# Performance work log

Hardware: AMD Instinct MI355X
Metric: run time of the kernel (lower is better)

## Reference

```python
import jax, jax.numpy as jnp
import numpy as np

N_HEAD_FULL = 16  # config.n_head

def setup_inputs() -> dict:
    key = jax.random.key(0)
    ks = jax.random.split(key, 5)
    B, T, D = 2, 2048, 2048
    s = 0.02
    return {
        "x": jax.random.normal(ks[0], (B, T, D), dtype=jnp.float32),
        "Wq": jax.random.normal(ks[1], (D, D), dtype=jnp.float32) * s,
        "Wk": jax.random.normal(ks[2], (D, D), dtype=jnp.float32) * s,
        "Wv": jax.random.normal(ks[3], (D, D), dtype=jnp.float32) * s,
        "Wo": jax.random.normal(ks[4], (D, D), dtype=jnp.float32) * s,
        "active_dim": 1024,
        "active_kv": 64,
    }

def reference(x, Wq, Wk, Wv, Wo, active_dim, active_kv):
    B, T, D = x.shape
    d = active_dim if active_dim is not None else D
    head_dim_base = D // N_HEAD_FULL          # 128
    kv_dim = active_kv if active_kv is not None else head_dim_base
    n_head = d // head_dim_base               # active heads
    head_dim = d // n_head                    # == head_dim_base

    xs = x[..., :d]                            # [B,T,d]
    # F.linear(x, W[:d,:d]) == x @ W[:d,:d].T
    q = jnp.einsum('btc,dc->btd', xs, Wq[:d, :d])
    k = jnp.einsum('btc,dc->btd', xs, Wk[:d, :d])
    v = jnp.einsum('btc,dc->btd', xs, Wv[:d, :d])

    def split_heads(t):  # [B,T,d] -> [B,h,T,hd]
        return t.reshape(B, T, n_head, head_dim).transpose(0, 2, 1, 3)
    q, k, v = split_heads(q), split_heads(k), split_heads(v)

    if kv_dim < head_dim:
        q, k, v = q[..., :kv_dim], k[..., :kv_dim], v[..., :kv_dim]

    scale = 1.0 / np.sqrt(kv_dim).astype(np.float32)
    attn = jnp.einsum('bhqd,bhkd->bhqk', q, k) * scale  # [B,h,T,T]
    causal = jnp.tril(jnp.ones((T, T), dtype=bool))
    attn = jnp.where(causal, attn, jnp.float32(-jnp.inf))
    attn = jax.nn.softmax(attn, axis=-1)
    out = jnp.einsum('bhqk,bhkd->bhqd', attn, v)        # [B,h,T,kv]

    if kv_dim < head_dim:
        out = jnp.pad(out, ((0, 0), (0, 0), (0, 0), (0, head_dim - kv_dim)))
    out = out.transpose(0, 2, 1, 3).reshape(B, T, d)
    out = jnp.einsum('btc,dc->btd', out, Wo[:d, :d])
    if d < D:
        out = jnp.pad(out, ((0, 0), (0, 0), (0, D - d)))
    return out
```

## Files before the change

kernel.cpp:

```cpp
#include <hip/hip_runtime.h>
#include <hip/hip_bf16.h>

typedef __attribute__((ext_vector_type(8))) short bf16x8;
typedef __attribute__((ext_vector_type(4))) float f32x4;

#define MFMA16(a,b,c) __builtin_amdgcn_mfma_f32_16x16x32_bf16((a),(b),(c),0,0,0)

static __device__ __forceinline__ unsigned short f2bf(float f) {
    unsigned int u = __builtin_bit_cast(unsigned int, f);
    u += 0x7fffu + ((u >> 16) & 1u);
    return (unsigned short)(u >> 16);
}

static __device__ __forceinline__ void g2l16(const unsigned short* g, unsigned short* l) {
    __builtin_amdgcn_global_load_lds(
        (const __attribute__((address_space(1))) unsigned int*)g,
        (__attribute__((address_space(3))) unsigned int*)l,
        16, 0, 0);
}

#define BT     4096
#define DFULL  2048
#define DACT   1024
#define DKV    64
#define NSEL   512
#define TSEQ   2048
#define PADR   72

__global__ __launch_bounds__(256) void prep_kernel(
    const float* __restrict__ x,  const float* __restrict__ Wq,
    const float* __restrict__ Wk, const float* __restrict__ Wv,
    const float* __restrict__ Wo,
    unsigned short* __restrict__ xb,  unsigned short* __restrict__ Wqb,
    unsigned short* __restrict__ Wkb, unsigned short* __restrict__ Wvb,
    unsigned short* __restrict__ Wob)
{
    const int NA = (BT * DACT) / 8;
    const int NB = (NSEL * DACT) / 8;
    const int NC = (DACT * NSEL) / 8;
    const int TOT = NA + 3 * NB + NC;
    for (int u = blockIdx.x * blockDim.x + threadIdx.x; u < TOT;
         u += gridDim.x * blockDim.x) {
        if (u < NA) {
            int e = u * 8; int row = e >> 10, col = e & 1023;
            const float* s = x + (size_t)row * DFULL + col;
            f32x4 v0 = *(const f32x4*)s, v1 = *(const f32x4*)(s + 4);
            bf16x8 o;
            #pragma unroll
            for (int j = 0; j < 4; ++j) { o[j] = (short)f2bf(v0[j]); o[4+j] = (short)f2bf(v1[j]); }
            *(bf16x8*)(xb + e) = o;
        } else if (u < NA + 3 * NB) {
            int t = u - NA; int mat = t / NB; int q = t % NB;
            int e = q * 8; int n = e >> 10, c = e & 1023;
            const float* W = (mat == 0) ? Wq : (mat == 1) ? Wk : Wv;
            unsigned short* Wb = (mat == 0) ? Wqb : (mat == 1) ? Wkb : Wvb;
            int wrow = (n >> 6) * 128 + (n & 63);
            const float* s = W + (size_t)wrow * DFULL + c;
            f32x4 v0 = *(const f32x4*)s, v1 = *(const f32x4*)(s + 4);
            bf16x8 o;
            #pragma unroll
            for (int j = 0; j < 4; ++j) { o[j] = (short)f2bf(v0[j]); o[4+j] = (short)f2bf(v1[j]); }
            *(bf16x8*)(Wb + e) = o;
        } else {
            int q = u - NA - 3 * NB;
            int e = q * 8; int r = e >> 9, cs = e & 511;
            int col = (cs >> 6) * 128 + (cs & 63);
            const float* s = Wo + (size_t)r * DFULL + col;
            f32x4 v0 = *(const f32x4*)s, v1 = *(const f32x4*)(s + 4);
            bf16x8 o;
            #pragma unroll
            for (int j = 0; j < 4; ++j) { o[j] = (short)f2bf(v0[j]); o[4+j] = (short)f2bf(v1[j]); }
            *(bf16x8*)(Wob + e) = o;
        }
    }
}

__global__ __launch_bounds__(256) void qkv_gemm(
    const unsigned short* __restrict__ xb,
    const unsigned short* __restrict__ Wall,
    unsigned short* __restrict__ Qb, unsigned short* __restrict__ Kb,
    unsigned short* __restrict__ Vtb)
{
    __shared__ unsigned short As[64 * 64];
    __shared__ unsigned short Bs[128 * 64];
    const int m0 = blockIdx.y * 64, n0 = blockIdx.x * 128;
    const int tid = threadIdx.x, w = tid >> 6, l = tid & 63;
    const int lr = l & 15, g = l >> 4, lk = g * 8;
    const int wr = w >> 1, wc = w & 1;
    const int srow = l >> 3, scol = (l & 7) * 8;

    f32x4 acc[2][4] = {};
    for (int k0 = 0; k0 < DACT; k0 += 64) {
        __syncthreads();
        #pragma unroll
        for (int i = 0; i < 2; ++i) {
            int chunk = w * 2 + i;
            int row = chunk * 8 + srow;
            g2l16(&xb[(size_t)(m0 + row) * DACT + k0 + scol], &As[chunk * 512]);
        }
        #pragma unroll
        for (int i = 0; i < 4; ++i) {
            int chunk = w * 4 + i;
            int row = chunk * 8 + srow;
            g2l16(&Wall[(size_t)(n0 + row) * DACT + k0 + scol], &Bs[chunk * 512]);
        }
        __syncthreads();
        #pragma unroll
        for (int kk = 0; kk < 64; kk += 32) {
            bf16x8 a[2], b[4];
            #pragma unroll
            for (int m = 0; m < 2; ++m)
                a[m] = *(const bf16x8*)&As[(wr * 32 + m * 16 + lr) * 64 + kk + lk];
            #pragma unroll
            for (int n = 0; n < 4; ++n)
                b[n] = *(const bf16x8*)&Bs[(wc * 64 + n * 16 + lr) * 64 + kk + lk];
            #pragma unroll
            for (int m = 0; m < 2; ++m)
                #pragma unroll
                for (int n = 0; n < 4; ++n)
                    acc[m][n] = MFMA16(a[m], b[n], acc[m][n]);
        }
    }
    #pragma unroll
    for (int m = 0; m < 2; ++m)
        #pragma unroll
        for (int n = 0; n < 4; ++n)
            #pragma unroll
            for (int i = 0; i < 4; ++i) {
                int row = m0 + wr * 32 + m * 16 + g * 4 + i;
                int col = n0 + wc * 64 + n * 16 + lr;
                int mat = col >> 9, r = col & 511, h = r >> 6, j = r & 63;
                int bb = row >> 11, t = row & 2047, bh = bb * 8 + h;
                float v = acc[m][n][i];
                if (mat == 0)
                    Qb[((size_t)bh * TSEQ + t) * DKV + j] = f2bf(v * 0.125f);
                else if (mat == 1)
                    Kb[((size_t)bh * TSEQ + t) * DKV + (j ^ ((t & 7) << 3))] = f2bf(v);
                else
                    Vtb[(((size_t)bh * 32 + (t >> 6)) * 64 + j) * 64 +
                        ((t & 63) ^ ((j & 7) << 3))] = f2bf(v);
            }
}

__global__ __launch_bounds__(512, 4) void attn_kernel(
    const unsigned short* __restrict__ Qb,
    const unsigned short* __restrict__ Kb,
    const unsigned short* __restrict__ Vtb,
    unsigned short* __restrict__ att)
{
    __shared__ unsigned short KV[2][2][2][4096];
    __shared__ unsigned short Ps[8][16 * 64];
    const int f = blockIdx.x;
    const int k = f & 255, bh = k & 15, pi = k >> 4;
    const int S = (f < 256) ? (31 - pi) : pi;
    const int ntt = S + 1;
    const int np = (ntt + 1) >> 1;
    const int tid = threadIdx.x, w = tid >> 6, l = tid & 63;
    const int lr = l & 15, g = l >> 4, lk = g * 8;
    const int s = w >> 1, j = w & 1;
    const size_t kvb = (size_t)bh * TSEQ * DKV;
    const int bb = bh >> 3, h = bh & 7;
    const int qs0 = S * 64 + s * 16;

    unsigned short* Psw = Ps[w];
    const short os = (short)0x3F80;
    const bf16x8 ones = {os, os, os, os, os, os, os, os};

    bf16x8 qf0 = *(const bf16x8*)&Qb[kvb + (size_t)(qs0 + lr) * DKV + lk];
    bf16x8 qf1 = *(const bf16x8*)&Qb[kvb + (size_t)(qs0 + lr) * DKV + 32 + lk];

    f32x4 acc[4] = {};
    f32x4 dacc = {};

    #define STAGE(b, p)                                                        \
        do {                                                                   \
            int r_ = w >> 1, par_ = r_ >> 1, kv_ = r_ & 1;                     \
            int t_ = 2 * (p) + par_;                                           \
            if (t_ < ntt) {                                                    \
                const unsigned short* src_ =                                   \
                    (kv_ ? Vtb : Kb) + kvb + (size_t)t_ * 4096 + (w & 1) * 2048; \
                unsigned short* dst_ = &KV[b][par_][kv_][(w & 1) * 2048];      \
                g2l16(&src_[l * 8],        dst_);                              \
                g2l16(&src_[512 + l * 8],  dst_ + 512);                        \
                g2l16(&src_[1024 + l * 8], dst_ + 1024);                       \
                g2l16(&src_[1536 + l * 8], dst_ + 1536);                       \
            }                                                                  \
        } while (0)

    STAGE(0, 0);
    __syncthreads();

    for (int p = 0; p < np; ++p) {
        const int cur = p & 1;
        if (p + 1 < np) STAGE(cur ^ 1, p + 1);

        const int jt = 2 * p + j;
        if (jt < ntt) {
            const unsigned short* Kt = KV[cur][j][0];
            const unsigned short* Vt = KV[cur][j][1];

            #pragma unroll
            for (int c = 0; c < 4; ++c) {
                const int row = c * 16 + lr, sr = (row & 7) << 3;
                bf16x8 b0 = *(const bf16x8*)&Kt[row * 64 + (lk ^ sr)];
                bf16x8 b1 = *(const bf16x8*)&Kt[row * 64 + ((32 + lk) ^ sr)];
                f32x4 z = {};
                z = MFMA16(qf0, b0, z);
                z = MFMA16(qf1, b1, z);
                if (jt == ntt - 1) {
                    int kcol = jt * 64 + c * 16 + lr;
                    #pragma unroll
                    for (int i = 0; i < 4; ++i)
                        if (kcol > qs0 + g * 4 + i) z[i] = -64.f;
                }
                const int colp = c * 16 + lr;
                #pragma unroll
                for (int i = 0; i < 4; ++i) {
                    const int prow = g * 4 + i;
                    Psw[prow * 64 + (colp ^ ((prow & 7) << 3))] =
                        f2bf(__expf(z[i]));
                }
            }
            const int psr = (lr & 7) << 3;
            bf16x8 pa0 = *(const bf16x8*)&Psw[lr * 64 + (lk ^ psr)];
            bf16x8 pa1 = *(const bf16x8*)&Psw[lr * 64 + ((32 + lk) ^ psr)];

            #pragma unroll
            for (int n = 0; n < 4; ++n) {
                const int row = n * 16 + lr, sr = (row & 7) << 3;
                bf16x8 v0 = *(const bf16x8*)&Vt[row * 64 + (lk ^ sr)];
                bf16x8 v1 = *(const bf16x8*)&Vt[row * 64 + ((32 + lk) ^ sr)];
                acc[n] = MFMA16(pa0, v0, acc[n]);
                acc[n] = MFMA16(pa1, v1, acc[n]);
            }
            dacc = MFMA16(pa0, ones, dacc);
            dacc = MFMA16(pa1, ones, dacc);
        }
        __syncthreads();
    }
    #undef STAGE

    float* M = (float*)KV;
    if (j == 1) {
        #pragma unroll
        for (int n = 0; n < 4; ++n)
            #pragma unroll
            for (int i = 0; i < 4; ++i)
                M[s * 1088 + (g * 4 + i) * 64 + n * 16 + lr] = acc[n][i];
        if (lr == 0) {
            #pragma unroll
            for (int i = 0; i < 4; ++i)
                M[s * 1088 + 1024 + g * 4 + i] = dacc[i];
        }
    }
    __syncthreads();
    if (j == 0) {
        #pragma unroll
        for (int i = 0; i < 4; ++i) {
            float den = dacc[i] + M[s * 1088 + 1024 + g * 4 + i];
            float inv = 1.0f / den;
            int t = qs0 + g * 4 + i;
            #pragma unroll
            for (int n = 0; n < 4; ++n) {
                float v = acc[n][i] + M[s * 1088 + (g * 4 + i) * 64 + n * 16 + lr];
                att[((size_t)bb * TSEQ + t) * NSEL + h * 64 + n * 16 + lr] =
                    f2bf(v * inv);
            }
        }
    }
}

__global__ __launch_bounds__(256) void oproj_gemm(
    const unsigned short* __restrict__ att,
    const unsigned short* __restrict__ Wob,
    float* __restrict__ out)
{
    const int tid = threadIdx.x;
    if (blockIdx.x >= 8) {
        const int m0z = blockIdx.y * 128;
        const int n0z = DACT + (blockIdx.x - 8) * 128;
        const f32x4 z = {0.f, 0.f, 0.f, 0.f};
        #pragma unroll
        for (int i = 0; i < 16; ++i) {
            int chunk = tid + i * 256;
            int row = chunk >> 5, c = (chunk & 31) * 4;
            *(f32x4*)&out[(size_t)(m0z + row) * DFULL + n0z + c] = z;
        }
        return;
    }
    __shared__ unsigned short As[128 * 64];
    __shared__ unsigned short Bs[128 * 64];
    const int m0 = blockIdx.y * 128, n0 = blockIdx.x * 128;
    const int w = tid >> 6, l = tid & 63;
    const int lr = l & 15, g = l >> 4, lk = g * 8;
    const int wr = w >> 1, wc = w & 1;
    const int srow = l >> 3, scol = (l & 7) * 8;

    f32x4 acc[4][4] = {};
    for (int k0 = 0; k0 < NSEL; k0 += 64) {
        __syncthreads();
        #pragma unroll
        for (int i = 0; i < 4; ++i) {
            int chunk = w * 4 + i;
            int row = chunk * 8 + srow;
            g2l16(&att[(size_t)(m0 + row) * NSEL + k0 + scol], &As[chunk * 512]);
            g2l16(&Wob[(size_t)(n0 + row) * NSEL + k0 + scol], &Bs[chunk * 512]);
        }
        __syncthreads();
        #pragma unroll
        for (int kk = 0; kk < 64; kk += 32) {
            bf16x8 a[4], b[4];
            #pragma unroll
            for (int m = 0; m < 4; ++m)
                a[m] = *(const bf16x8*)&As[(wr * 64 + m * 16 + lr) * 64 + kk + lk];
            #pragma unroll
            for (int n = 0; n < 4; ++n)
                b[n] = *(const bf16x8*)&Bs[(wc * 64 + n * 16 + lr) * 64 + kk + lk];
            #pragma unroll
            for (int m = 0; m < 4; ++m)
                #pragma unroll
                for (int n = 0; n < 4; ++n)
                    acc[m][n] = MFMA16(a[m], b[n], acc[m][n]);
        }
    }
    #pragma unroll
    for (int m = 0; m < 4; ++m)
        #pragma unroll
        for (int n = 0; n < 4; ++n)
            #pragma unroll
            for (int i = 0; i < 4; ++i) {
                int row = m0 + wr * 64 + m * 16 + g * 4 + i;
                int col = n0 + wc * 64 + n * 16 + lr;
                out[(size_t)row * DFULL + col] = acc[m][n][i];
            }
}

extern "C" void kernel_launch(void* const* d_in, const int* in_sizes, int n_in,
                              void* d_out, int out_size, void* d_ws, size_t ws_size,
                              hipStream_t stream) {
    const float* x  = (const float*)d_in[0];
    const float* Wq = (const float*)d_in[1];
    const float* Wk = (const float*)d_in[2];
    const float* Wv = (const float*)d_in[3];
    const float* Wo = (const float*)d_in[4];
    float* out = (float*)d_out;

    char* ws = (char*)d_ws;
    unsigned short* xb  = (unsigned short*)(ws);
    unsigned short* Wqb = (unsigned short*)(ws + 8388608);
    unsigned short* Wkb = (unsigned short*)(ws + 9437184);
    unsigned short* Wvb = (unsigned short*)(ws + 10485760);
    unsigned short* Wob = (unsigned short*)(ws + 11534336);
    unsigned short* Qb  = (unsigned short*)(ws + 12582912);
    unsigned short* Kb  = (unsigned short*)(ws + 16777216);
    unsigned short* Vtb = (unsigned short*)(ws + 20971520);
    unsigned short* att = (unsigned short*)(ws + 25165824);

    prep_kernel<<<2048, 256, 0, stream>>>(x, Wq, Wk, Wv, Wo,
                                          xb, Wqb, Wkb, Wvb, Wob);
    qkv_gemm<<<dim3(12, 64), 256, 0, stream>>>(xb, Wqb, Qb, Kb, Vtb);
    attn_kernel<<<512, 512, 0, stream>>>(Qb, Kb, Vtb, att);
    oproj_gemm<<<dim3(16, 32), 256, 0, stream>>>(att, Wob, out);
}
```

Baseline: 82.57 us.

## Halve attention query tile to 32 rows with 4-wave blocks

Splits each attention block's 64-row query tile into two 32-row tiles run by 256-thread blocks, doubling the grid to 1024 blocks. Each wave now stages a full K or V tile through two LDS halves, and the compute loops pick the half by row. The aim is better load balance and occupancy across CUs for the causal triangle. The cost is that K/V tiles are streamed from memory twice as often per query row.

```diff
diff --git a/kernel.cpp b/kernel.cpp
--- a/kernel.cpp
+++ b/kernel.cpp
@@ -142,25 +142,26 @@
             }
 }
 
-__global__ __launch_bounds__(512, 4) void attn_kernel(
+__global__ __launch_bounds__(256, 4) void attn_kernel(
     const unsigned short* __restrict__ Qb,
     const unsigned short* __restrict__ Kb,
     const unsigned short* __restrict__ Vtb,
     unsigned short* __restrict__ att)
 {
-    __shared__ unsigned short KV[2][2][2][4096];
-    __shared__ unsigned short Ps[8][16 * 64];
+    __shared__ unsigned short KV[2][2][2][2048];
+    __shared__ unsigned short KV2[2][2][2][2048];
+    __shared__ unsigned short Ps[4][16 * 64];
     const int f = blockIdx.x;
-    const int k = f & 255, bh = k & 15, pi = k >> 4;
-    const int S = (f < 256) ? (31 - pi) : pi;
-    const int ntt = S + 1;
+    const int k = f & 511, bh = k & 15, pi = k >> 4;
+    const int Q = (f < 512) ? (63 - pi) : pi;
+    const int ntt = (Q >> 1) + 1;
     const int np = (ntt + 1) >> 1;
     const int tid = threadIdx.x, w = tid >> 6, l = tid & 63;
     const int lr = l & 15, g = l >> 4, lk = g * 8;
     const int s = w >> 1, j = w & 1;
     const size_t kvb = (size_t)bh * TSEQ * DKV;
     const int bb = bh >> 3, h = bh & 7;
-    const int qs0 = S * 64 + s * 16;
+    const int qs0 = Q * 32 + s * 16;
 
     unsigned short* Psw = Ps[w];
     const short os = (short)0x3F80;
@@ -174,16 +175,21 @@
 
     #define STAGE(b, p)                                                        \
         do {                                                                   \
-            int r_ = w >> 1, par_ = r_ >> 1, kv_ = r_ & 1;                     \
+            int par_ = w >> 1, kv_ = w & 1;                                    \
             int t_ = 2 * (p) + par_;                                           \
             if (t_ < ntt) {                                                    \
                 const unsigned short* src_ =                                   \
-                    (kv_ ? Vtb : Kb) + kvb + (size_t)t_ * 4096 + (w & 1) * 2048; \
-                unsigned short* dst_ = &KV[b][par_][kv_][(w & 1) * 2048];      \
-                g2l16(&src_[l * 8],        dst_);                              \
-                g2l16(&src_[512 + l * 8],  dst_ + 512);                        \
-                g2l16(&src_[1024 + l * 8], dst_ + 1024);                       \
-                g2l16(&src_[1536 + l * 8], dst_ + 1536);                       \
+                    (kv_ ? Vtb : Kb) + kvb + (size_t)t_ * 4096;                \
+                unsigned short* d0_ = KV[b][par_][kv_];                        \
+                unsigned short* d1_ = KV2[b][par_][kv_];                       \
+                g2l16(&src_[l * 8],        d0_);                               \
+                g2l16(&src_[512 + l * 8],  d0_ + 512);                         \
+                g2l16(&src_[1024 + l * 8], d0_ + 1024);                        \
+                g2l16(&src_[1536 + l * 8], d0_ + 1536);                        \
+                g2l16(&src_[2048 + l * 8], d1_);                               \
+                g2l16(&src_[2560 + l * 8], d1_ + 512);                         \
+                g2l16(&src_[3072 + l * 8], d1_ + 1024);                        \
+                g2l16(&src_[3584 + l * 8], d1_ + 1536);                        \
             }                                                                  \
         } while (0)
 
@@ -196,14 +202,18 @@
 
         const int jt = 2 * p + j;
         if (jt < ntt) {
-            const unsigned short* Kt = KV[cur][j][0];
-            const unsigned short* Vt = KV[cur][j][1];
+            const unsigned short* Kt0 = KV[cur][j][0];
+            const unsigned short* Kt1 = KV2[cur][j][0];
+            const unsigned short* Vt0 = KV[cur][j][1];
+            const unsigned short* Vt1 = KV2[cur][j][1];
 
             #pragma unroll
             for (int c = 0; c < 4; ++c) {
                 const int row = c * 16 + lr, sr = (row & 7) << 3;
-                bf16x8 b0 = *(const bf16x8*)&Kt[row * 64 + (lk ^ sr)];
-                bf16x8 b1 = *(const bf16x8*)&Kt[row * 64 + ((32 + lk) ^ sr)];
+                const unsigned short* Kt = (row < 32) ? Kt0 : Kt1;
+                const int rrow = row & 31;
+                bf16x8 b0 = *(const bf16x8*)&Kt[rrow * 64 + (lk ^ sr)];
+                bf16x8 b1 = *(const bf16x8*)&Kt[rrow * 64 + ((32 + lk) ^ sr)];
                 f32x4 z = {};
                 z = MFMA16(qf0, b0, z);
                 z = MFMA16(qf1, b1, z);
@@ -228,8 +238,10 @@
             #pragma unroll
             for (int n = 0; n < 4; ++n) {
                 const int row = n * 16 + lr, sr = (row & 7) << 3;
-                bf16x8 v0 = *(const bf16x8*)&Vt[row * 64 + (lk ^ sr)];
-                bf16x8 v1 = *(const bf16x8*)&Vt[row * 64 + ((32 + lk) ^ sr)];
+                const unsigned short* Vt = (row < 32) ? Vt0 : Vt1;
+                const int rrow = row & 31;
+                bf16x8 v0 = *(const bf16x8*)&Vt[rrow * 64 + (lk ^ sr)];
+                bf16x8 v1 = *(const bf16x8*)&Vt[rrow * 64 + ((32 + lk) ^ sr)];
                 acc[n] = MFMA16(pa0, v0, acc[n]);
                 acc[n] = MFMA16(pa1, v1, acc[n]);
             }
@@ -359,6 +371,6 @@
     prep_kernel<<<2048, 256, 0, stream>>>(x, Wq, Wk, Wv, Wo,
                                           xb, Wqb, Wkb, Wvb, Wob);
     qkv_gemm<<<dim3(12, 64), 256, 0, stream>>>(xb, Wqb, Qb, Kb, Vtb);
-    attn_kernel<<<512, 512, 0, stream>>>(Qb, Kb, Vtb, att);
+    attn_kernel<<<1024, 256, 0, stream>>>(Qb, Kb, Vtb, att);
     oproj_gemm<<<dim3(16, 32), 256, 0, stream>>>(att, Wob, out);
 }
```

New measurement: 93.56 us. +13.3%, slower.

## Split attention blocks into 32-row query tiles and drop LDS double buffering

Applied to the files above, without the earlier changes.

The attention kernel now launches 1024 blocks of 256 threads, each covering 32 query rows instead of 64, so there are twice as many smaller blocks. The LDS K/V double buffer becomes a single buffer, loaded synchronously each iteration with barriers before and after the load. This halves LDS per block, which should let more blocks fit per CU and spread the causal workload more evenly. The cost is that K/V tiles are reloaded by twice as many blocks, and load latency is no longer overlapped with compute.

```diff
diff --git a/kernel.cpp b/kernel.cpp
--- a/kernel.cpp
+++ b/kernel.cpp
@@ -142,25 +142,25 @@
             }
 }
 
-__global__ __launch_bounds__(512, 4) void attn_kernel(
+__global__ __launch_bounds__(256, 4) void attn_kernel(
     const unsigned short* __restrict__ Qb,
     const unsigned short* __restrict__ Kb,
     const unsigned short* __restrict__ Vtb,
     unsigned short* __restrict__ att)
 {
-    __shared__ unsigned short KV[2][2][2][4096];
-    __shared__ unsigned short Ps[8][16 * 64];
+    __shared__ unsigned short KV[2][2][4096];
+    __shared__ unsigned short Ps[4][16 * 64];
     const int f = blockIdx.x;
-    const int k = f & 255, bh = k & 15, pi = k >> 4;
-    const int S = (f < 256) ? (31 - pi) : pi;
-    const int ntt = S + 1;
+    const int k = f & 511, bh = k & 15, pi = k >> 4;
+    const int Q = (f < 512) ? (63 - pi) : pi;
+    const int ntt = (Q >> 1) + 1;
     const int np = (ntt + 1) >> 1;
     const int tid = threadIdx.x, w = tid >> 6, l = tid & 63;
     const int lr = l & 15, g = l >> 4, lk = g * 8;
     const int s = w >> 1, j = w & 1;
     const size_t kvb = (size_t)bh * TSEQ * DKV;
     const int bb = bh >> 3, h = bh & 7;
-    const int qs0 = S * 64 + s * 16;
+    const int qs0 = Q * 32 + s * 16;
 
     unsigned short* Psw = Ps[w];
     const short os = (short)0x3F80;
@@ -172,32 +172,34 @@
     f32x4 acc[4] = {};
     f32x4 dacc = {};
 
-    #define STAGE(b, p)                                                        \
+    #define STAGE(p)                                                           \
         do {                                                                   \
-            int r_ = w >> 1, par_ = r_ >> 1, kv_ = r_ & 1;                     \
+            int par_ = w >> 1, kv_ = w & 1;                                    \
             int t_ = 2 * (p) + par_;                                           \
             if (t_ < ntt) {                                                    \
                 const unsigned short* src_ =                                   \
-                    (kv_ ? Vtb : Kb) + kvb + (size_t)t_ * 4096 + (w & 1) * 2048; \
-                unsigned short* dst_ = &KV[b][par_][kv_][(w & 1) * 2048];      \
-                g2l16(&src_[l * 8],        dst_);                              \
-                g2l16(&src_[512 + l * 8],  dst_ + 512);                        \
-                g2l16(&src_[1024 + l * 8], dst_ + 1024);                       \
-                g2l16(&src_[1536 + l * 8], dst_ + 1536);                       \
+                    (kv_ ? Vtb : Kb) + kvb + (size_t)t_ * 4096;                \
+                unsigned short* d_ = KV[par_][kv_];                            \
+                g2l16(&src_[l * 8],        d_);                                \
+                g2l16(&src_[512 + l * 8],  d_ + 512);                          \
+                g2l16(&src_[1024 + l * 8], d_ + 1024);                         \
+                g2l16(&src_[1536 + l * 8], d_ + 1536);                         \
+                g2l16(&src_[2048 + l * 8], d_ + 2048);                         \
+                g2l16(&src_[2560 + l * 8], d_ + 2560);                         \
+                g2l16(&src_[3072 + l * 8], d_ + 3072);                         \
+                g2l16(&src_[3584 + l * 8], d_ + 3584);                         \
             }                                                                  \
         } while (0)
 
-    STAGE(0, 0);
-    __syncthreads();
-
     for (int p = 0; p < np; ++p) {
-        const int cur = p & 1;
-        if (p + 1 < np) STAGE(cur ^ 1, p + 1);
+        __syncthreads();
+        STAGE(p);
+        __syncthreads();
 
         const int jt = 2 * p + j;
         if (jt < ntt) {
-            const unsigned short* Kt = KV[cur][j][0];
-            const unsigned short* Vt = KV[cur][j][1];
+            const unsigned short* Kt = KV[j][0];
+            const unsigned short* Vt = KV[j][1];
 
             #pragma unroll
             for (int c = 0; c < 4; ++c) {
@@ -236,9 +238,9 @@
             dacc = MFMA16(pa0, ones, dacc);
             dacc = MFMA16(pa1, ones, dacc);
         }
-        __syncthreads();
     }
     #undef STAGE
+    __syncthreads();
 
     float* M = (float*)KV;
     if (j == 1) {
@@ -359,6 +361,6 @@
     prep_kernel<<<2048, 256, 0, stream>>>(x, Wq, Wk, Wv, Wo,
                                           xb, Wqb, Wkb, Wvb, Wob);
     qkv_gemm<<<dim3(12, 64), 256, 0, stream>>>(xb, Wqb, Qb, Kb, Vtb);
-    attn_kernel<<<512, 512, 0, stream>>>(Qb, Kb, Vtb, att);
+    attn_kernel<<<1024, 256, 0, stream>>>(Qb, Kb, Vtb, att);
     oproj_gemm<<<dim3(16, 32), 256, 0, stream>>>(att, Wob, out);
 }
```

Result: no change. 82.04 us (-0.6%).
